# Kernel tuning notes

Measured on AMD Instinct MI355X. Metric: run time of the kernel, lower is better.

Reference implementation:

```python
import jax, jax.numpy as jnp
import numpy as np

S_DIM = 4096
N_NODES = 4096
N_EDGES = 32768


def _coarsen(ei_np, N):
    """Integer-only greedy coarsening, faithful to MNGRAPH.forward's while-loop.
    Returns (select order, flattened neighbor indices, segment ids, per-hub
    neighbor counts, forward-fill indices replicating the stale-M behavior for
    empty neighborhoods, and the remapped final edge_index)."""
    ei = ei_np.astype(np.int64).copy()
    I = np.bincount(ei[0], minlength=N)
    O = np.bincount(ei[1], minlength=N)
    order = np.argsort(-(I + O), kind='stable')  # torch.argsort(D, descending=True)
    visits = np.zeros(N, dtype=bool)
    select = []
    nbr_idx, nbr_seg, counts = [], [], []
    while order.size > 0:
        node = int(order[0])
        select.append(node)
        visits[node] = True
        # H = unique neighbors of node in the CURRENT (rewritten) edge_index
        H = np.unique(np.concatenate([ei[1][ei[0] == node], ei[0][ei[1] == node]]))
        visits[H] = True
        order = order[~visits[order]]
        # rewrite: endpoints in H that are not already-selected hubs -> node
        Hn = H[~np.isin(H, np.asarray(select, dtype=np.int64))]
        ei[np.isin(ei, Hn)] = node
        ei = ei[:, ei[0] != ei[1]]  # drop self-loops
        # append reversed edges that are not already present (pair-code isin
        # == the original O(E^2) all/any comparison, computed efficiently)
        code = ei[0] * N + ei[1]
        rcode = ei[1] * N + ei[0]
        new = ~np.isin(rcode, code)
        ei = np.concatenate([ei, ei[::-1][:, new]], axis=1)
        k = len(select) - 1
        nbr_idx.append(H)
        nbr_seg.append(np.full(H.shape[0], k, dtype=np.int64))
        counts.append(H.shape[0])
    select = np.asarray(select, dtype=np.int64)
    sort_sel = np.sort(select)
    ei_out = np.searchsorted(sort_sel, ei)  # compact node ids
    counts = np.asarray(counts, dtype=np.int64)
    # forward-fill: when H is empty the original appends the previous (stale) M
    fill = np.arange(select.shape[0])
    for i in range(select.shape[0]):
        if counts[i] == 0:
            fill[i] = fill[i - 1] if i > 0 else 0
    nbr = np.concatenate(nbr_idx) if nbr_idx else np.zeros(0, np.int64)
    seg = np.concatenate(nbr_seg) if nbr_seg else np.zeros(0, np.int64)
    return select, nbr, seg, counts, fill, ei_out


def setup_inputs() -> dict:
    key = jax.random.key(0)
    k1, k2, k3, k4 = jax.random.split(key, 4)
    x = jax.random.normal(k1, (N_NODES, S_DIM), dtype=jnp.float32)
    edge_index = jax.random.randint(k2, (2, N_EDGES), 0, N_NODES, dtype=jnp.int64)
    bound = float(np.sqrt(6.0 / (1.0 + S_DIM)))  # xavier_uniform on (1, S)
    W1 = jax.random.uniform(k3, (S_DIM,), jnp.float32, -bound, bound)
    W2 = jax.random.uniform(k4, (S_DIM,), jnp.float32, -bound, bound)
    B1 = jnp.zeros((S_DIM,), jnp.float32)
    B2 = jnp.zeros((S_DIM,), jnp.float32)
    return {"x": x, "edge_index": edge_index, "W1": W1, "W2": W2, "B1": B1, "B2": B2}


def reference(x, edge_index, W1, W2, B1, B2):
    N = x.shape[0]
    sel, nbr, seg, counts, fill, ei_out = _coarsen(np.asarray(edge_index), N)
    K = sel.shape[0]
    # Dn = x[n]*W1+B1 for every neighbor of every hub; per-hub mean via segment_sum
    Dn = x[jnp.asarray(nbr)] * W1 + B1                      # [T, S]
    sums = jax.ops.segment_sum(Dn, jnp.asarray(seg), num_segments=K)
    denom = jnp.maximum(jnp.asarray(counts), 1).astype(x.dtype)[:, None]
    mean_Dn = sums / denom                                  # [K, S]
    Dv = x[jnp.asarray(sel)] * W2 + B2                      # [K, S]
    END = jnp.concatenate([Dv, mean_Dn], axis=1)            # [K, 2S]
    END = END[jnp.asarray(fill)]                            # stale-M replication
    return END, jnp.asarray(ei_out)
```

## Files before the change

### kernel.cpp

```cpp
#include <hip/hip_runtime.h>
#include <hip/hip_bf16.h>

#define NT 512
#define NW (NT / 64)
#define NNODES 4096
#define ECAP 65536

__global__ __launch_bounds__(256)
void zeroBM(int4* __restrict__ bm) {
    bm[(size_t)blockIdx.x * 256 + threadIdx.x] = make_int4(0, 0, 0, 0);
}

__device__ __forceinline__ int blockScanExcl(int v, int* s_w, int* total) {
    const int tid  = threadIdx.x;
    const int lane = tid & 63;
    const int wv   = tid >> 6;
    int x = v;
#pragma unroll
    for (int off = 1; off < 64; off <<= 1) {
        int t = __shfl_up(x, off, 64);
        if (lane >= off) x += t;
    }
    if (lane == 63) s_w[wv] = x;
    __syncthreads();
    if (tid < 16) {
        int y = (tid < NW) ? s_w[tid] : 0;
#pragma unroll
        for (int off = 1; off < 16; off <<= 1) {
            int t = __shfl_up(y, off, 16);
            if (tid >= off) y += t;
        }
        s_w[tid] = y;
    }
    __syncthreads();
    int base = wv ? s_w[wv - 1] : 0;
    int tot  = s_w[15];
    __syncthreads();
    *total = tot;
    return base + x - v;
}

__global__ __launch_bounds__(NT, 1)
void phaseA(const int* __restrict__ ei, int E0,
            int* __restrict__ U, int* __restrict__ V,
            unsigned int* __restrict__ BM,
            int* __restrict__ NBR, int* __restrict__ OTH,
            int* __restrict__ SEL, int* __restrict__ CNTS,
            int* __restrict__ NST, int* __restrict__ FIL, int* __restrict__ SC,
            int* __restrict__ TMP, float* __restrict__ out)
{
    __shared__ unsigned short s_ord[NNODES];
    __shared__ unsigned short s_pos[NNODES];
    __shared__ unsigned short s_so[NNODES];
    __shared__ unsigned char  s_rank[NNODES];
    __shared__ unsigned int   s_visbits[NNODES / 32];
    __shared__ unsigned int   s_hb[NNODES / 32];
    __shared__ unsigned int   s_meta[NNODES];
    __shared__ int s_mat[64][65];
    __shared__ int s_roff[NNODES];
    __shared__ int s_rend[NNODES];
    __shared__ int s_stamp[NNODES];
    __shared__ int s_degcnt[NNODES];
    __shared__ int s_w[16];
    __shared__ int s_bc[16];

    const int tid = threadIdx.x;

    for (int i = tid; i < NNODES; i += NT) s_degcnt[i] = 0;
    for (int i = tid; i < NNODES / 32; i += NT) { s_hb[i] = 0u; s_visbits[i] = 0u; }
    if (tid < 16) s_bc[tid] = 0;
    __syncthreads();

    for (int i = tid; i < E0; i += NT)
        if (ei[2 * i + 1] != 0) s_bc[9] = 1;
    __syncthreads();
    const int is64 = !s_bc[9];

    for (int e = tid; e < E0; e += NT) {
        int uu = ei[is64 ? 2 * e : e];
        int vv = ei[is64 ? 2 * (E0 + e) : (E0 + e)];
        U[e] = uu; V[e] = vv;
        atomicAdd(&s_degcnt[uu], 1);
        atomicAdd(&s_degcnt[vv], 1);
    }
    __syncthreads();
    for (int n = tid; n < NNODES; n += NT) atomicMax(&s_bc[7], s_degcnt[n]);
    __syncthreads();
    const int maxd = s_bc[7];

    if (maxd < 64) {
        const int wv = tid >> 6, lane = tid & 63;
        const unsigned long long wltm = (1ull << lane) - 1ull;
        for (int g = wv; g < 64; g += NW) {
            int n = g * 64 + lane;
            int d = s_degcnt[n];
            int rk = 0;
            for (int dd = 0; dd < 64; ++dd) {
                unsigned long long bal = __ballot(d == dd);
                if (lane == 0) s_mat[dd][g] = __popcll(bal);
                if (d == dd) rk = __popcll(bal & wltm);
            }
            s_rank[n] = (unsigned char)rk;
        }
        __syncthreads();
        if (tid < 64) {
            int run = 0;
            for (int g = 0; g < 64; ++g) { int t = s_mat[tid][g]; s_mat[tid][g] = run; run += t; }
            s_mat[tid][64] = run;
        }
        __syncthreads();
        if (tid < 64) {
            int x = s_mat[tid][64];
#pragma unroll
            for (int off = 1; off < 64; off <<= 1) {
                int t = __shfl_up(x, off, 64);
                if (tid >= off) x += t;
            }
            int T = __shfl(x, 63, 64);
            s_mat[tid][64] = T - x;
        }
        __syncthreads();
        for (int g = wv; g < 64; g += NW) {
            int n = g * 64 + lane;
            int d = s_degcnt[n];
            int pos = s_mat[d][64] + s_mat[d][g] + (int)s_rank[n];
            s_ord[pos] = (unsigned short)n;
        }
        __syncthreads();
    } else {
        for (int d = maxd; d >= 0; --d) {
            const int n0 = tid * 8;
            int f[8], cnt = 0;
#pragma unroll
            for (int q = 0; q < 8; ++q) { f[q] = (s_degcnt[n0 + q] == d); cnt += f[q]; }
            int tot;
            int off = blockScanExcl(cnt, s_w, &tot);
            int idx = s_bc[4] + off;
#pragma unroll
            for (int q = 0; q < 8; ++q)
                if (f[q]) s_ord[idx++] = (unsigned short)(n0 + q);
            __syncthreads();
            if (tid == 0) s_bc[4] += tot;
            __syncthreads();
        }
    }

    for (int i = tid; i < NNODES; i += NT) s_pos[s_ord[i]] = (unsigned short)i;
    __syncthreads();

    if (tid == 0) {
        s_bc[0] = (int)s_ord[0];
        atomicOr(&s_visbits[0], 1u);
    }
    __syncthreads();
    {
        const int node = s_bc[0];
        for (int e = tid; e < E0; e += NT) {
            int uu = U[e], vv = V[e];
            if (uu == node) {
                int w = vv; unsigned m = 1u << (w & 31);
                unsigned old = atomicOr(&s_hb[w >> 5], m);
                if (!(old & m)) {
                    int i = atomicAdd(&s_bc[2], 1);
                    s_degcnt[i] = w;
                    int sl = (int)s_pos[w];
                    atomicOr(&s_visbits[sl >> 5], 1u << (sl & 31));
                }
            }
            if (vv == node) {
                int w = uu; unsigned m = 1u << (w & 31);
                unsigned old = atomicOr(&s_hb[w >> 5], m);
                if (!(old & m)) {
                    int i = atomicAdd(&s_bc[2], 1);
                    s_degcnt[i] = w;
                    int sl = (int)s_pos[w];
                    atomicOr(&s_visbits[sl >> 5], 1u << (sl & 31));
                }
            }
        }
        __syncthreads();
        for (int e = tid; e < E0; e += NT) {
            int uu = U[e];
            if (uu != node && ((s_hb[uu >> 5] >> (uu & 31)) & 1)) U[e] = node;
            int vv = V[e];
            if (vv != node && ((s_hb[vv >> 5] >> (vv & 31)) & 1)) V[e] = node;
        }
        __syncthreads();
    }

    for (int e = tid; e < E0; e += NT) {
        int uu = U[e], vv = V[e];
        if (uu != vv) {
            unsigned code = ((unsigned)uu << 12) | (unsigned)vv;
            atomicOr(&BM[code >> 5], 1u << (code & 31));
        }
    }
    __syncthreads();
    for (int t0 = 0; t0 < E0; t0 += NT * 32) {
        unsigned fm = 0u;
        const int base = t0 + tid * 32;
        for (int j = 0; j < 32; ++j) {
            int e = base + j;
            if (e < E0) {
                int uu = U[e], vv = V[e];
                if (uu != vv) {
                    unsigned rc = ((unsigned)vv << 12) | (unsigned)uu;
                    unsigned old = atomicOr(&BM[rc >> 5], 0u);
                    if (!((old >> (rc & 31)) & 1u)) fm |= (1u << j);
                }
            }
        }
        int tot;
        int off = blockScanExcl(__popc(fm), s_w, &tot);
        int r = s_bc[5] + off;
        unsigned m = fm;
        while (m) {
            int j = __ffs((int)m) - 1; m &= m - 1;
            int e = base + j;
            U[E0 + r] = V[e]; V[E0 + r] = U[e];
            ++r;
        }
        __syncthreads();
        if (tid == 0) s_bc[5] += tot;
        __syncthreads();
    }
    const int E1 = E0 + s_bc[5];

    for (int n = tid; n < NNODES; n += NT) s_roff[n] = 0;
    __syncthreads();
    for (int e = tid; e < E1; e += NT) {
        int uu = U[e], vv = V[e];
        if (uu != vv) atomicAdd(&s_roff[uu], 1);
    }
    __syncthreads();
    {
        const int n0 = tid * 8;
        int c[8], s = 0;
#pragma unroll
        for (int q = 0; q < 8; ++q) { c[q] = s_roff[n0 + q]; s += c[q]; }
        int tot;
        int off = blockScanExcl(s, s_w, &tot);
        int st = off;
#pragma unroll
        for (int q = 0; q < 8; ++q) {
            s_roff[n0 + q] = st; s_rend[n0 + q] = st; st += c[q];
        }
    }
    __syncthreads();
    for (int e = tid; e < E1; e += NT) {
        int uu = U[e], vv = V[e];
        if (uu != vv) {
            int p = atomicAdd(&s_rend[uu], 1);
            OTH[p] = vv;
        }
    }
    __syncthreads();
    const int cnt0 = s_bc[2];
    for (int i = tid; i < cnt0; i += NT) NBR[i] = s_degcnt[i];
    __syncthreads();

    for (int i = tid; i < NNODES; i += NT) {
        int nd = (int)s_ord[i];
        s_meta[nd] = ((unsigned)i << 16) | (unsigned)nd;
        s_stamp[i] = 0;
        s_degcnt[i] = 0;
    }
    __syncthreads();
    if (tid == 0) {
        int hub0 = s_bc[0];
        s_meta[hub0] = (unsigned)hub0 | 0x8000u;
        s_so[0] = (unsigned short)hub0;
        s_degcnt[0] = cnt0;
    }
    __syncthreads();

    if (tid < 64) {
        const int ln = tid;
        const unsigned long long ltm = (1ull << ln) - 1ull;
        volatile int* vstamp = s_stamp;

        int nc = cnt0;
        int k = 1;

        unsigned lo = 0u, hi = 0u;
        auto extract = [&]() -> int {
            unsigned long long b = __ballot(lo != 0u);
            if (b) {
                int sl = __ffsll((long long)b) - 1;
                unsigned ww = __shfl(lo, sl, 64);
                if (ln == sl) lo &= lo - 1;
                return sl * 32 + (__ffs((int)ww) - 1);
            }
            b = __ballot(hi != 0u);
            if (b) {
                int sl = __ffsll((long long)b) - 1;
                unsigned ww = __shfl(hi, sl, 64);
                if (ln == sl) hi &= hi - 1;
                return 2048 + sl * 32 + (__ffs((int)ww) - 1);
            }
            return -1;
        };

        auto commitNew = [&](unsigned g, int w, bool nw, unsigned long long bal,
                             unsigned relv) {
            if (nw) {
                NBR[nc + __popcll(bal & ltm)] = w;
                int slot = (int)(g >> 16);
                atomicOr(&s_visbits[slot >> 5], 1u << (slot & 31));
                if (!(g & 0x8000u)) s_meta[w] = relv;
            }
            nc += __popcll(bal);
        };

        auto procFast = [&](int hub, int hslot, int o, unsigned g) {
            const unsigned relv = ((unsigned)hslot << 16) | (unsigned)hub | 0x8000u;
            int w = (o >= 0) ? (int)(g & 0x7FFFu) : hub;
            bool valid = (o >= 0) && (w != hub);
            if (valid) vstamp[w] = ln;
            int r = valid ? vstamp[w] : -1;
            bool nw = valid && (r == ln);
            unsigned long long bal = __ballot(nw);
            commitNew(g, w, nw, bal, relv);
        };

        auto procSlow = [&](int hub, int hslot, int rb, int re, int o0) {
            const unsigned relv = ((unsigned)hslot << 16) | (unsigned)hub | 0x8000u;
            const int key = k << 6;
            int o = o0;
            for (int s0 = rb; s0 < re; s0 += 64) {
                unsigned g = (o >= 0) ? s_meta[o] : 0u;
                int w = (o >= 0) ? (int)(g & 0x7FFFu) : hub;
                bool cnd = (w != hub);
                int old = key;
                if (cnd) old = atomicMax(&s_stamp[w], key);
                bool nw = cnd && (old < key);
                unsigned long long bal = __ballot(nw);
                commitNew(g, w, nw, bal, relv);
                int s1 = s0 + 64;
                o = (s1 + ln < re) ? OTH[s1 + ln] : -1;
            }
        };

        for (;;) {
            lo = ~s_visbits[ln]; hi = ~s_visbits[ln + 64];
            int sl0 = extract();
            if (sl0 < 0) break;
            int sl1 = extract(), sl2 = -1, sl3 = -1;
            if (sl1 >= 0) { sl2 = extract(); if (sl2 >= 0) sl3 = extract(); }

            int c0 = (int)s_ord[sl0];
            int c1 = (sl1 >= 0) ? (int)s_ord[sl1] : -1;
            int c2 = (sl2 >= 0) ? (int)s_ord[sl2] : -1;
            int c3 = (sl3 >= 0) ? (int)s_ord[sl3] : -1;

            {
                int ms = (ln == 0) ? sl0 : (ln == 1) ? sl1 : (ln == 2) ? sl2 : sl3;
                if (ln < 4 && ms >= 0) atomicOr(&s_visbits[ms >> 5], 1u << (ms & 31));
            }

            int rb0 = s_roff[c0], re0 = s_rend[c0];
            int rb1 = 0, re1 = 0, rb2 = 0, re2 = 0, rb3 = 0, re3 = 0;
            if (c1 >= 0) { rb1 = s_roff[c1]; re1 = s_rend[c1]; }
            if (c2 >= 0) { rb2 = s_roff[c2]; re2 = s_rend[c2]; }
            if (c3 >= 0) { rb3 = s_roff[c3]; re3 = s_rend[c3]; }
            int v0 = (rb0 + ln < re0) ? OTH[rb0 + ln] : -1;
            int v1 = (c1 >= 0 && rb1 + ln < re1) ? OTH[rb1 + ln] : -1;
            int v2 = (c2 >= 0 && rb2 + ln < re2) ? OTH[rb2 + ln] : -1;
            int v3 = (c3 >= 0 && rb3 + ln < re3) ? OTH[rb3 + ln] : -1;

            if (ln == 0) {
                s_meta[c0] = ((unsigned)sl0 << 16) | (unsigned)c0 | 0x8000u;
                s_so[k] = (unsigned short)c0;
            }
            {
                unsigned g0 = (v0 >= 0) ? s_meta[v0] : 0u;
                int begin = nc;
                if (re0 - rb0 <= 64) procFast(c0, sl0, v0, g0);
                else                 procSlow(c0, sl0, rb0, re0, v0);
                if (ln == 0) s_degcnt[k] = nc - begin;
                k++;
            }
            if (c1 >= 0) {
                unsigned m1 = s_meta[c1];
                unsigned g1 = (v1 >= 0) ? s_meta[v1] : 0u;
                if ((int)(m1 & 0x7FFFu) == c1) {
                    if (ln == 0) {
                        s_meta[c1] = ((unsigned)sl1 << 16) | (unsigned)c1 | 0x8000u;
                        s_so[k] = (unsigned short)c1;
                    }
                    int begin = nc;
                    if (re1 - rb1 <= 64) procFast(c1, sl1, v1, g1);
                    else                 procSlow(c1, sl1, rb1, re1, v1);
                    if (ln == 0) s_degcnt[k] = nc - begin;
                    k++;
                }
            }
            if (c2 >= 0) {
                unsigned m2 = s_meta[c2];
                unsigned g2 = (v2 >= 0) ? s_meta[v2] : 0u;
                if ((int)(m2 & 0x7FFFu) == c2) {
                    if (ln == 0) {
                        s_meta[c2] = ((unsigned)sl2 << 16) | (unsigned)c2 | 0x8000u;
                        s_so[k] = (unsigned short)c2;
                    }
                    int begin = nc;
                    if (re2 - rb2 <= 64) procFast(c2, sl2, v2, g2);
                    else                 procSlow(c2, sl2, rb2, re2, v2);
                    if (ln == 0) s_degcnt[k] = nc - begin;
                    k++;
                }
            }
            if (c3 >= 0) {
                unsigned m3 = s_meta[c3];
                unsigned g3 = (v3 >= 0) ? s_meta[v3] : 0u;
                if ((int)(m3 & 0x7FFFu) == c3) {
                    if (ln == 0) {
                        s_meta[c3] = ((unsigned)sl3 << 16) | (unsigned)c3 | 0x8000u;
                        s_so[k] = (unsigned short)c3;
                    }
                    int begin = nc;
                    if (re3 - rb3 <= 64) procFast(c3, sl3, v3, g3);
                    else                 procSlow(c3, sl3, rb3, re3, v3);
                    if (ln == 0) s_degcnt[k] = nc - begin;
                    k++;
                }
            }
        }
        const int K = k;

        {
            int base = 0;
            for (int c = 0; c < NNODES / 64; ++c) {
                int n = c * 64 + ln;
                unsigned mv = s_meta[n];
                int f = ((mv & 0x8000u) != 0u) && ((int)(mv & 0x7FFFu) == n);
                unsigned long long b = __ballot(f);
                s_stamp[n] = base + __popcll(b & ltm);
                base += __popcll(b);
            }
        }
        {
            int nb = 0;
            for (int c = 0; c * 64 < K; ++c) {
                int i = c * 64 + ln;
                int cv = (i < K) ? s_degcnt[i] : 0;
                int x = cv;
#pragma unroll
                for (int off = 1; off < 64; off <<= 1) {
                    int t = __shfl_up(x, off, 64);
                    if (ln >= off) x += t;
                }
                if (i < K) { NST[i] = nb + x - cv; CNTS[i] = cv; SEL[i] = (int)s_so[i]; }
                nb += __shfl(x, 63, 64);
            }
        }
        {
            int carry = 0;
            for (int c = 0; c * 64 < K; ++c) {
                int i = c * 64 + ln;
                int f = (i < K) && (s_degcnt[i] > 0);
                unsigned long long b = __ballot(f);
                unsigned long long m = b & ((ln == 63) ? ~0ull : ((1ull << (ln + 1)) - 1ull));
                int fil = m ? (c * 64 + 63 - __clzll(m)) : carry;
                if (i < K) FIL[i] = fil;
                carry = b ? (c * 64 + 63 - __clzll(b)) : carry;
            }
        }
        if (ln == 0) { SC[0] = K; s_bc[3] = K; }
    }
    __syncthreads();

    const int K = s_bc[3];
    const size_t obase = (size_t)K * 8192;

    for (int t0 = 0; t0 < E1; t0 += NT * 64) {
        unsigned long long fm = 0ull;
        const int base = t0 + tid * 64;
        if (base + 64 <= E1) {
            const int4* U4 = (const int4*)(U + base);
            const int4* V4 = (const int4*)(V + base);
#pragma unroll
            for (int q = 0; q < 16; ++q) {
                int4 a = U4[q], b = V4[q];
                int j = q * 4;
                if ((s_meta[a.x] ^ s_meta[b.x]) & 0x7FFFu) fm |= 1ull << j;
                if ((s_meta[a.y] ^ s_meta[b.y]) & 0x7FFFu) fm |= 1ull << (j + 1);
                if ((s_meta[a.z] ^ s_meta[b.z]) & 0x7FFFu) fm |= 1ull << (j + 2);
                if ((s_meta[a.w] ^ s_meta[b.w]) & 0x7FFFu) fm |= 1ull << (j + 3);
            }
        } else {
            for (int j = 0; j < 64; ++j) {
                int e = base + j;
                if (e < E1) {
                    if ((s_meta[U[e]] ^ s_meta[V[e]]) & 0x7FFFu) fm |= 1ull << j;
                }
            }
        }
        int tot;
        int off = blockScanExcl(__popcll(fm), s_w, &tot);
        int r = s_bc[10] + off;
        unsigned long long m = fm;
        while (m) {
            int j = __ffsll((long long)m) - 1; m &= m - 1;
            int e = base + j;
            out[obase + (size_t)r] = (float)s_stamp[(int)(s_meta[U[e]] & 0x7FFFu)];
            TMP[r] = s_stamp[(int)(s_meta[V[e]] & 0x7FFFu)];
            ++r;
        }
        __syncthreads();
        if (tid == 0) s_bc[10] += tot;
        __syncthreads();
    }
    const int Ef = s_bc[10];
    if (tid == 0) SC[1] = Ef;
    for (int r = tid; r < Ef; r += NT)
        out[obase + (size_t)Ef + (size_t)r] = (float)TMP[r];
}

__global__ __launch_bounds__(256, 4)
void phaseB(const float* __restrict__ x,
            const float* __restrict__ W1, const float* __restrict__ W2,
            const float* __restrict__ B1, const float* __restrict__ B2,
            const int* __restrict__ NBR, const int* __restrict__ SEL,
            const int* __restrict__ CNTS, const int* __restrict__ NST,
            const int* __restrict__ FIL, const int* __restrict__ SC,
            float* __restrict__ out)
{
    const int K = SC[0];
    const int k = blockIdx.x;
    if (k >= K) return;
    const int kk   = FIL[k];
    const int node = SEL[kk];
    const int cnt  = CNTS[kk];
    const int st   = NST[kk];
    const int tid  = threadIdx.x;
    const float4* x4 = (const float4*)x;

    float4 acc[4];
#pragma unroll
    for (int j = 0; j < 4; j++) acc[j] = make_float4(0.f, 0.f, 0.f, 0.f);

    for (int r = 0; r < cnt; ++r) {
        const float4* row = x4 + (size_t)NBR[st + r] * 1024;
#pragma unroll
        for (int j = 0; j < 4; j++) {
            float4 t = row[tid + j * 256];
            acc[j].x += t.x; acc[j].y += t.y; acc[j].z += t.z; acc[j].w += t.w;
        }
    }

    const float fc  = (float)cnt;
    const float inv = 1.0f / (float)(cnt > 1 ? cnt : 1);
    const float4* xr = x4 + (size_t)node * 1024;
    float4* o4 = (float4*)(out + (size_t)k * 8192);

#pragma unroll
    for (int j = 0; j < 4; j++) {
        int c = tid + j * 256;
        float4 w1 = ((const float4*)W1)[c], b1 = ((const float4*)B1)[c];
        float4 w2 = ((const float4*)W2)[c], b2 = ((const float4*)B2)[c];
        float4 xv = xr[c];
        float4 pd, pm;
        pd.x = xv.x * w2.x + b2.x;
        pd.y = xv.y * w2.y + b2.y;
        pd.z = xv.z * w2.z + b2.z;
        pd.w = xv.w * w2.w + b2.w;
        pm.x = (acc[j].x * w1.x + fc * b1.x) * inv;
        pm.y = (acc[j].y * w1.y + fc * b1.y) * inv;
        pm.z = (acc[j].z * w1.z + fc * b1.z) * inv;
        pm.w = (acc[j].w * w1.w + fc * b1.w) * inv;
        o4[c] = pd;
        o4[1024 + c] = pm;
    }
}

extern "C" void kernel_launch(void* const* d_in, const int* in_sizes, int n_in,
                              void* d_out, int out_size, void* d_ws, size_t ws_size,
                              hipStream_t stream)
{
    const float* x  = (const float*)d_in[0];
    const int*   ei = (const int*)d_in[1];
    const float* W1 = (const float*)d_in[2];
    const float* W2 = (const float*)d_in[3];
    const float* B1 = (const float*)d_in[4];
    const float* B2 = (const float*)d_in[5];
    const int E0 = in_sizes[1] / 2;

    char* w = (char*)d_ws;
    int* U = (int*)w;
    int* V = U + ECAP;
    unsigned int* BM = (unsigned int*)(V + ECAP);
    int* OTH = (int*)BM;
    int* NBR = OTH + 2 * ECAP;
    int* TMP = NBR + 2 * ECAP;
    char* meta = (char*)BM + (2u << 20);
    int* SEL   = (int*)meta;
    int* CNTS  = SEL  + NNODES;
    int* NST   = CNTS + NNODES;
    int* FIL   = NST  + NNODES;
    int* SC    = FIL  + NNODES;
    float* out = (float*)d_out;

    hipLaunchKernelGGL(zeroBM, dim3(512), dim3(256), 0, stream, (int4*)BM);

    hipLaunchKernelGGL(phaseA, dim3(1), dim3(NT), 0, stream,
                       ei, E0, U, V, BM, NBR, OTH,
                       SEL, CNTS, NST, FIL, SC, TMP, out);

    hipLaunchKernelGGL(phaseB, dim3(NNODES), dim3(256), 0, stream,
                       x, W1, W2, B1, B2, NBR, SEL, CNTS, NST, FIL, SC, out);
}
```

Before: 1.039 ms.

## Replace global edge bitmap with shared-memory CSR lookup and double block size

Removes the 2MB global bitmap (and its zeroing kernel) used to detect existing reverse edges. Instead it builds a per-source CSR of targets in LDS, held in a union that reuses shared storage from later phases, and checks reverse edges by linear scan over the target list. The single-block phaseA goes from 512 to 1024 threads, with the scan helpers adjusted to 4 nodes per thread. This avoids a kernel launch and global atomics, at the cost of scans that grow with degree and of the 16-wave scan limit now being fully used.

```diff
diff --git a/kernel.cpp b/kernel.cpp
--- a/kernel.cpp
+++ b/kernel.cpp
@@ -1,15 +1,10 @@
 #include <hip/hip_runtime.h>
 #include <hip/hip_bf16.h>
 
-#define NT 512
+#define NT 1024
 #define NW (NT / 64)
 #define NNODES 4096
 #define ECAP 65536
-
-__global__ __launch_bounds__(256)
-void zeroBM(int4* __restrict__ bm) {
-    bm[(size_t)blockIdx.x * 256 + threadIdx.x] = make_int4(0, 0, 0, 0);
-}
 
 __device__ __forceinline__ int blockScanExcl(int v, int* s_w, int* total) {
     const int tid  = threadIdx.x;
@@ -24,7 +19,7 @@
     if (lane == 63) s_w[wv] = x;
     __syncthreads();
     if (tid < 16) {
-        int y = (tid < NW) ? s_w[tid] : 0;
+        int y = s_w[tid];
 #pragma unroll
         for (int off = 1; off < 16; off <<= 1) {
             int t = __shfl_up(y, off, 16);
@@ -43,7 +38,6 @@
 __global__ __launch_bounds__(NT, 1)
 void phaseA(const int* __restrict__ ei, int E0,
             int* __restrict__ U, int* __restrict__ V,
-            unsigned int* __restrict__ BM,
             int* __restrict__ NBR, int* __restrict__ OTH,
             int* __restrict__ SEL, int* __restrict__ CNTS,
             int* __restrict__ NST, int* __restrict__ FIL, int* __restrict__ SC,
@@ -52,15 +46,20 @@
     __shared__ unsigned short s_ord[NNODES];
     __shared__ unsigned short s_pos[NNODES];
     __shared__ unsigned short s_so[NNODES];
-    __shared__ unsigned char  s_rank[NNODES];
     __shared__ unsigned int   s_visbits[NNODES / 32];
     __shared__ unsigned int   s_hb[NNODES / 32];
-    __shared__ unsigned int   s_meta[NNODES];
-    __shared__ int s_mat[64][65];
     __shared__ int s_roff[NNODES];
     __shared__ int s_rend[NNODES];
-    __shared__ int s_stamp[NNODES];
     __shared__ int s_degcnt[NNODES];
+    __shared__ union {
+        struct {
+            int mat[64][65];
+            unsigned char rank[NNODES];
+            int stamp[NNODES];
+            unsigned int meta[NNODES];
+        } a;
+        unsigned short tgt[ECAP / 2];
+    } uP;
     __shared__ int s_w[16];
     __shared__ int s_bc[16];
 
@@ -97,48 +96,48 @@
             int rk = 0;
             for (int dd = 0; dd < 64; ++dd) {
                 unsigned long long bal = __ballot(d == dd);
-                if (lane == 0) s_mat[dd][g] = __popcll(bal);
+                if (lane == 0) uP.a.mat[dd][g] = __popcll(bal);
                 if (d == dd) rk = __popcll(bal & wltm);
             }
-            s_rank[n] = (unsigned char)rk;
+            uP.a.rank[n] = (unsigned char)rk;
         }
         __syncthreads();
         if (tid < 64) {
             int run = 0;
-            for (int g = 0; g < 64; ++g) { int t = s_mat[tid][g]; s_mat[tid][g] = run; run += t; }
-            s_mat[tid][64] = run;
+            for (int g = 0; g < 64; ++g) { int t = uP.a.mat[tid][g]; uP.a.mat[tid][g] = run; run += t; }
+            uP.a.mat[tid][64] = run;
         }
         __syncthreads();
         if (tid < 64) {
-            int x = s_mat[tid][64];
+            int x = uP.a.mat[tid][64];
 #pragma unroll
             for (int off = 1; off < 64; off <<= 1) {
                 int t = __shfl_up(x, off, 64);
                 if (tid >= off) x += t;
             }
             int T = __shfl(x, 63, 64);
-            s_mat[tid][64] = T - x;
+            uP.a.mat[tid][64] = T - x;
         }
         __syncthreads();
         for (int g = wv; g < 64; g += NW) {
             int n = g * 64 + lane;
             int d = s_degcnt[n];
-            int pos = s_mat[d][64] + s_mat[d][g] + (int)s_rank[n];
+            int pos = uP.a.mat[d][64] + uP.a.mat[d][g] + (int)uP.a.rank[n];
             s_ord[pos] = (unsigned short)n;
         }
         __syncthreads();
     } else {
         for (int d = maxd; d >= 0; --d) {
-            const int n0 = tid * 8;
-            int f[8], cnt = 0;
-#pragma unroll
-            for (int q = 0; q < 8; ++q) { f[q] = (s_degcnt[n0 + q] == d); cnt += f[q]; }
+            int n0 = tid * 4;
+            int f0 = (s_degcnt[n0] == d), f1 = (s_degcnt[n0 + 1] == d);
+            int f2 = (s_degcnt[n0 + 2] == d), f3 = (s_degcnt[n0 + 3] == d);
             int tot;
-            int off = blockScanExcl(cnt, s_w, &tot);
+            int off = blockScanExcl(f0 + f1 + f2 + f3, s_w, &tot);
             int idx = s_bc[4] + off;
-#pragma unroll
-            for (int q = 0; q < 8; ++q)
-                if (f[q]) s_ord[idx++] = (unsigned short)(n0 + q);
+            if (f0) s_ord[idx++] = (unsigned short)n0;
+            if (f1) s_ord[idx++] = (unsigned short)(n0 + 1);
+            if (f2) s_ord[idx++] = (unsigned short)(n0 + 2);
+            if (f3) s_ord[idx++] = (unsigned short)(n0 + 3);
             __syncthreads();
             if (tid == 0) s_bc[4] += tot;
             __syncthreads();
@@ -188,11 +187,30 @@
         __syncthreads();
     }
 
+    for (int n = tid; n < NNODES; n += NT) s_roff[n] = 0;
+    __syncthreads();
+    for (int e = tid; e < E0; e += NT) {
+        int uu = U[e], vv = V[e];
+        if (uu != vv) atomicAdd(&s_roff[uu], 1);
+    }
+    __syncthreads();
+    {
+        const int n0 = tid * 4;
+        int c0 = s_roff[n0], c1 = s_roff[n0 + 1], c2 = s_roff[n0 + 2], c3 = s_roff[n0 + 3];
+        int tot;
+        int off = blockScanExcl(c0 + c1 + c2 + c3, s_w, &tot);
+        int st = off;
+        s_roff[n0] = st;     s_rend[n0] = st;     st += c0;
+        s_roff[n0 + 1] = st; s_rend[n0 + 1] = st; st += c1;
+        s_roff[n0 + 2] = st; s_rend[n0 + 2] = st; st += c2;
+        s_roff[n0 + 3] = st; s_rend[n0 + 3] = st;
+    }
+    __syncthreads();
     for (int e = tid; e < E0; e += NT) {
         int uu = U[e], vv = V[e];
         if (uu != vv) {
-            unsigned code = ((unsigned)uu << 12) | (unsigned)vv;
-            atomicOr(&BM[code >> 5], 1u << (code & 31));
+            int p = atomicAdd(&s_rend[uu], 1);
+            uP.tgt[p] = (unsigned short)vv;
         }
     }
     __syncthreads();
@@ -204,9 +222,11 @@
             if (e < E0) {
                 int uu = U[e], vv = V[e];
                 if (uu != vv) {
-                    unsigned rc = ((unsigned)vv << 12) | (unsigned)uu;
-                    unsigned old = atomicOr(&BM[rc >> 5], 0u);
-                    if (!((old >> (rc & 31)) & 1u)) fm |= (1u << j);
+                    bool found = false;
+                    int rb = s_roff[vv], re = s_rend[vv];
+                    for (int i = rb; i < re; ++i)
+                        if ((int)uP.tgt[i] == uu) { found = true; break; }
+                    if (!found) fm |= (1u << j);
                 }
             }
         }
@@ -234,17 +254,15 @@
     }
     __syncthreads();
     {
-        const int n0 = tid * 8;
-        int c[8], s = 0;
-#pragma unroll
-        for (int q = 0; q < 8; ++q) { c[q] = s_roff[n0 + q]; s += c[q]; }
+        const int n0 = tid * 4;
+        int c0 = s_roff[n0], c1 = s_roff[n0 + 1], c2 = s_roff[n0 + 2], c3 = s_roff[n0 + 3];
         int tot;
-        int off = blockScanExcl(s, s_w, &tot);
+        int off = blockScanExcl(c0 + c1 + c2 + c3, s_w, &tot);
         int st = off;
-#pragma unroll
-        for (int q = 0; q < 8; ++q) {
-            s_roff[n0 + q] = st; s_rend[n0 + q] = st; st += c[q];
-        }
+        s_roff[n0] = st;     s_rend[n0] = st;     st += c0;
+        s_roff[n0 + 1] = st; s_rend[n0 + 1] = st; st += c1;
+        s_roff[n0 + 2] = st; s_rend[n0 + 2] = st; st += c2;
+        s_roff[n0 + 3] = st; s_rend[n0 + 3] = st;
     }
     __syncthreads();
     for (int e = tid; e < E1; e += NT) {
@@ -261,14 +279,14 @@
 
     for (int i = tid; i < NNODES; i += NT) {
         int nd = (int)s_ord[i];
-        s_meta[nd] = ((unsigned)i << 16) | (unsigned)nd;
-        s_stamp[i] = 0;
+        uP.a.meta[nd] = ((unsigned)i << 16) | (unsigned)nd;
+        uP.a.stamp[i] = 0;
         s_degcnt[i] = 0;
     }
     __syncthreads();
     if (tid == 0) {
         int hub0 = s_bc[0];
-        s_meta[hub0] = (unsigned)hub0 | 0x8000u;
+        uP.a.meta[hub0] = (unsigned)hub0 | 0x8000u;
         s_so[0] = (unsigned short)hub0;
         s_degcnt[0] = cnt0;
     }
@@ -277,7 +295,7 @@
     if (tid < 64) {
         const int ln = tid;
         const unsigned long long ltm = (1ull << ln) - 1ull;
-        volatile int* vstamp = s_stamp;
+        volatile int* vstamp = uP.a.stamp;
 
         int nc = cnt0;
         int k = 1;
@@ -307,7 +325,7 @@
                 NBR[nc + __popcll(bal & ltm)] = w;
                 int slot = (int)(g >> 16);
                 atomicOr(&s_visbits[slot >> 5], 1u << (slot & 31));
-                if (!(g & 0x8000u)) s_meta[w] = relv;
+                if (!(g & 0x8000u)) uP.a.meta[w] = relv;
             }
             nc += __popcll(bal);
         };
@@ -328,11 +346,11 @@
             const int key = k << 6;
             int o = o0;
             for (int s0 = rb; s0 < re; s0 += 64) {
-                unsigned g = (o >= 0) ? s_meta[o] : 0u;
+                unsigned g = (o >= 0) ? uP.a.meta[o] : 0u;
                 int w = (o >= 0) ? (int)(g & 0x7FFFu) : hub;
                 bool cnd = (w != hub);
                 int old = key;
-                if (cnd) old = atomicMax(&s_stamp[w], key);
+                if (cnd) old = atomicMax(&uP.a.stamp[w], key);
                 bool nw = cnd && (old < key);
                 unsigned long long bal = __ballot(nw);
                 commitNew(g, w, nw, bal, relv);
@@ -369,11 +387,11 @@
             int v3 = (c3 >= 0 && rb3 + ln < re3) ? OTH[rb3 + ln] : -1;
 
             if (ln == 0) {
-                s_meta[c0] = ((unsigned)sl0 << 16) | (unsigned)c0 | 0x8000u;
+                uP.a.meta[c0] = ((unsigned)sl0 << 16) | (unsigned)c0 | 0x8000u;
                 s_so[k] = (unsigned short)c0;
             }
             {
-                unsigned g0 = (v0 >= 0) ? s_meta[v0] : 0u;
+                unsigned g0 = (v0 >= 0) ? uP.a.meta[v0] : 0u;
                 int begin = nc;
                 if (re0 - rb0 <= 64) procFast(c0, sl0, v0, g0);
                 else                 procSlow(c0, sl0, rb0, re0, v0);
@@ -381,11 +399,11 @@
                 k++;
             }
             if (c1 >= 0) {
-                unsigned m1 = s_meta[c1];
-                unsigned g1 = (v1 >= 0) ? s_meta[v1] : 0u;
+                unsigned m1 = uP.a.meta[c1];
+                unsigned g1 = (v1 >= 0) ? uP.a.meta[v1] : 0u;
                 if ((int)(m1 & 0x7FFFu) == c1) {
                     if (ln == 0) {
-                        s_meta[c1] = ((unsigned)sl1 << 16) | (unsigned)c1 | 0x8000u;
+                        uP.a.meta[c1] = ((unsigned)sl1 << 16) | (unsigned)c1 | 0x8000u;
                         s_so[k] = (unsigned short)c1;
                     }
                     int begin = nc;
@@ -396,11 +414,11 @@
                 }
             }
             if (c2 >= 0) {
-                unsigned m2 = s_meta[c2];
-                unsigned g2 = (v2 >= 0) ? s_meta[v2] : 0u;
+                unsigned m2 = uP.a.meta[c2];
+                unsigned g2 = (v2 >= 0) ? uP.a.meta[v2] : 0u;
                 if ((int)(m2 & 0x7FFFu) == c2) {
                     if (ln == 0) {
-                        s_meta[c2] = ((unsigned)sl2 << 16) | (unsigned)c2 | 0x8000u;
+                        uP.a.meta[c2] = ((unsigned)sl2 << 16) | (unsigned)c2 | 0x8000u;
                         s_so[k] = (unsigned short)c2;
                     }
                     int begin = nc;
@@ -411,11 +429,11 @@
                 }
             }
             if (c3 >= 0) {
-                unsigned m3 = s_meta[c3];
-                unsigned g3 = (v3 >= 0) ? s_meta[v3] : 0u;
+                unsigned m3 = uP.a.meta[c3];
+                unsigned g3 = (v3 >= 0) ? uP.a.meta[v3] : 0u;
                 if ((int)(m3 & 0x7FFFu) == c3) {
                     if (ln == 0) {
-                        s_meta[c3] = ((unsigned)sl3 << 16) | (unsigned)c3 | 0x8000u;
+                        uP.a.meta[c3] = ((unsigned)sl3 << 16) | (unsigned)c3 | 0x8000u;
                         s_so[k] = (unsigned short)c3;
                     }
                     int begin = nc;
@@ -432,10 +450,10 @@
             int base = 0;
             for (int c = 0; c < NNODES / 64; ++c) {
                 int n = c * 64 + ln;
-                unsigned mv = s_meta[n];
+                unsigned mv = uP.a.meta[n];
                 int f = ((mv & 0x8000u) != 0u) && ((int)(mv & 0x7FFFu) == n);
                 unsigned long long b = __ballot(f);
-                s_stamp[n] = base + __popcll(b & ltm);
+                uP.a.stamp[n] = base + __popcll(b & ltm);
                 base += __popcll(b);
             }
         }
@@ -483,16 +501,16 @@
             for (int q = 0; q < 16; ++q) {
                 int4 a = U4[q], b = V4[q];
                 int j = q * 4;
-                if ((s_meta[a.x] ^ s_meta[b.x]) & 0x7FFFu) fm |= 1ull << j;
-                if ((s_meta[a.y] ^ s_meta[b.y]) & 0x7FFFu) fm |= 1ull << (j + 1);
-                if ((s_meta[a.z] ^ s_meta[b.z]) & 0x7FFFu) fm |= 1ull << (j + 2);
-                if ((s_meta[a.w] ^ s_meta[b.w]) & 0x7FFFu) fm |= 1ull << (j + 3);
+                if ((uP.a.meta[a.x] ^ uP.a.meta[b.x]) & 0x7FFFu) fm |= 1ull << j;
+                if ((uP.a.meta[a.y] ^ uP.a.meta[b.y]) & 0x7FFFu) fm |= 1ull << (j + 1);
+                if ((uP.a.meta[a.z] ^ uP.a.meta[b.z]) & 0x7FFFu) fm |= 1ull << (j + 2);
+                if ((uP.a.meta[a.w] ^ uP.a.meta[b.w]) & 0x7FFFu) fm |= 1ull << (j + 3);
             }
         } else {
             for (int j = 0; j < 64; ++j) {
                 int e = base + j;
                 if (e < E1) {
-                    if ((s_meta[U[e]] ^ s_meta[V[e]]) & 0x7FFFu) fm |= 1ull << j;
+                    if ((uP.a.meta[U[e]] ^ uP.a.meta[V[e]]) & 0x7FFFu) fm |= 1ull << j;
                 }
             }
         }
@@ -503,8 +521,8 @@
         while (m) {
             int j = __ffsll((long long)m) - 1; m &= m - 1;
             int e = base + j;
-            out[obase + (size_t)r] = (float)s_stamp[(int)(s_meta[U[e]] & 0x7FFFu)];
-            TMP[r] = s_stamp[(int)(s_meta[V[e]] & 0x7FFFu)];
+            out[obase + (size_t)r] = (float)uP.a.stamp[(int)(uP.a.meta[U[e]] & 0x7FFFu)];
+            TMP[r] = uP.a.stamp[(int)(uP.a.meta[V[e]] & 0x7FFFu)];
             ++r;
         }
         __syncthreads();
@@ -587,24 +605,20 @@
     const int E0 = in_sizes[1] / 2;
 
     char* w = (char*)d_ws;
-    int* U = (int*)w;
-    int* V = U + ECAP;
-    unsigned int* BM = (unsigned int*)(V + ECAP);
-    int* OTH = (int*)BM;
+    int* U   = (int*)w;
+    int* V   = U + ECAP;
+    int* OTH = V + ECAP;
     int* NBR = OTH + 2 * ECAP;
     int* TMP = NBR + 2 * ECAP;
-    char* meta = (char*)BM + (2u << 20);
-    int* SEL   = (int*)meta;
+    int* SEL   = TMP + 2 * ECAP;
     int* CNTS  = SEL  + NNODES;
     int* NST   = CNTS + NNODES;
     int* FIL   = NST  + NNODES;
     int* SC    = FIL  + NNODES;
     float* out = (float*)d_out;
 
-    hipLaunchKernelGGL(zeroBM, dim3(512), dim3(256), 0, stream, (int4*)BM);
-
     hipLaunchKernelGGL(phaseA, dim3(1), dim3(NT), 0, stream,
-                       ei, E0, U, V, BM, NBR, OTH,
+                       ei, E0, U, V, NBR, OTH,
                        SEL, CNTS, NST, FIL, SC, TMP, out);
 
     hipLaunchKernelGGL(phaseB, dim3(NNODES), dim3(256), 0, stream,
```

Result: slower. 1.392 ms (+34.0%).
